# Optimization experiments

Hardware: AMD Instinct MI355X
Metric: run time of the kernel (lower is better)

The kernel has to match this reference:

```python
import jax, jax.numpy as jnp
import numpy as np

L, C, B = 256, 20, 1024


def _pos_mask(L):
    # pairwise mask: l2 - l1 >= 1, shape (L, L); broadcast over channels
    ls = jnp.arange(L)
    return (ls[None, :] - ls[:, None]) >= 1


def setup_inputs() -> dict:
    key = jax.random.key(0)
    k0, k1, k2 = jax.random.split(key, 3)
    x_lc = jax.random.uniform(k0, (B, L, C), dtype=jnp.float32)
    theta_0 = jnp.zeros((1,), dtype=jnp.float32)
    theta_lc = jax.random.normal(k1, (1, L, C), dtype=jnp.float32) / np.sqrt(L)
    pm = _pos_mask(L)
    theta_lclc = (jax.random.normal(k2, (1, L, C, L, C), dtype=jnp.float32)
                  / np.sqrt(L * L)) * pm[None, :, None, :, None]
    mask = pm
    return {"x_lc": x_lc, "theta_0": theta_0, "theta_lc": theta_lc,
            "theta_lclc": theta_lclc, "mask": mask}


def reference(x_lc, theta_0, theta_lc, theta_lclc, mask):
    Bn = x_lc.shape[0]
    # additive term: sum_{l,c} theta_lc * x
    phi = theta_0 + jnp.einsum('blc,zlc->b', x_lc, theta_lc)[:, None]
    # pairwise term as a masked bilinear form: x^T (mask * theta) x
    # (avoids materializing the (B,L,C,L,C) broadcast of the original)
    theta_m = theta_lclc[0] * mask[:, None, :, None].astype(theta_lclc.dtype)
    LC = L * C
    xf = x_lc.reshape(Bn, LC)                      # (B, LC)
    tf_ = theta_m.reshape(LC, LC)                  # (LC, LC)
    pair = jnp.einsum('bi,ij,bj->b', xf, tf_, xf)  # two GEMMs under the hood
    phi = phi + pair[:, None]
    return phi
```

## Files before the change

### kernel.cpp

```cpp
#include <hip/hip_runtime.h>
#include <stdint.h>

#define LDIM 256
#define CDIM 20
#define LC   5120
#define NB   1024
#define BM   256
#define BN   256
#define ITOT64 840

typedef __attribute__((ext_vector_type(8))) short short8;
typedef __attribute__((ext_vector_type(4))) float float4v;
typedef __attribute__((ext_vector_type(4))) unsigned int uint4v;
typedef unsigned short ushort_t;

#define TB_BYTES (52428800ull)
#define XB_BYTES (10485760ull)
#define WS_NEED  (TB_BYTES + XB_BYTES)

__device__ inline uint32_t pack_bf16x2(float a, float b) {
    uint32_t ua = __float_as_uint(a);
    uint32_t ub = __float_as_uint(b);
    ua += 0x7fffu + ((ua >> 16) & 1u);
    ub += 0x7fffu + ((ub >> 16) & 1u);
    return (ua >> 16) | (ub & 0xffff0000u);
}

__device__ inline float bf16_to_f32(ushort_t u) {
    return __uint_as_float(((uint32_t)u) << 16);
}

__device__ inline void load_lds16(const void* g, void* l) {
    __builtin_amdgcn_global_load_lds(
        (const __attribute__((address_space(1))) uint32_t*)g,
        (__attribute__((address_space(3))) uint32_t*)l, 16, 0, 0);
}

__global__ __launch_bounds__(256) void conv_kernel(
    const float* __restrict__ T, const float* __restrict__ X,
    const float* __restrict__ th0, const float* __restrict__ thlc,
    ushort_t* __restrict__ Tb, ushort_t* __restrict__ Xb,
    float* __restrict__ out)
{
    const int bid = blockIdx.x;
    const int t   = threadIdx.x;
    __shared__ float red[4];

    if (bid < LC) {
        const int r  = bid;
        const int tk = (r >> 8) << 8;
        const float*  src = T  + (size_t)r * LC;
        ushort_t*     dst = Tb + (size_t)r * LC;
        for (int c = tk + t * 4; c < LC; c += 1024) {
            float4 f = *(const float4*)(src + c);
            uint2 u;
            u.x = pack_bf16x2(f.x, f.y);
            u.y = pack_bf16x2(f.z, f.w);
            *(uint2*)(dst + c) = u;
        }
    } else {
        const int b = bid - LC;
        const float*  src = X  + (size_t)b * LC;
        ushort_t*     dst = Xb + (size_t)b * LC;
        float s = 0.f;
        for (int c = t * 4; c < LC; c += 1024) {
            float4 f = *(const float4*)(src + c);
            float4 w = *(const float4*)(thlc + c);
            s += f.x * w.x + f.y * w.y + f.z * w.z + f.w * w.w;
            uint2 u;
            u.x = pack_bf16x2(f.x, f.y);
            u.y = pack_bf16x2(f.z, f.w);
            *(uint2*)(dst + c) = u;
        }
        s += __shfl_xor(s, 1);  s += __shfl_xor(s, 2);  s += __shfl_xor(s, 4);
        s += __shfl_xor(s, 8);  s += __shfl_xor(s, 16); s += __shfl_xor(s, 32);
        if ((t & 63) == 0) red[t >> 6] = s;
        __syncthreads();
        if (t == 0) out[b] = th0[0] + red[0] + red[1] + red[2] + red[3];
    }
}

__global__ __launch_bounds__(512, 2) void pair_bf(
    const ushort_t* __restrict__ Tb, const ushort_t* __restrict__ Xb,
    float* __restrict__ out)
{
    const int n    = blockIdx.x;
    const int kblk = (n & 7) | ((n >> 5) << 3);
    const int bn0  = ((n >> 3) & 3) * BN;

    const int gbeg = (ITOT64 * kblk) >> 6;
    const int gend = (ITOT64 * (kblk + 1)) >> 6;

    int it = 0, pre = 0;
    while (pre + (80 - (it << 2)) <= gbeg) { pre += 80 - (it << 2); ++it; }
    int li = gbeg - pre;

    __shared__ __align__(16) ushort_t A_s[2048 * 8];
    __shared__ __align__(16) ushort_t B_s[2048 * 8];

    const int t    = threadIdx.x;
    const int lane = t & 63;
    const int wid  = t >> 6;
    const int wm   = (wid >> 1) * 64;
    const int wn   = (wid & 1) * 128;
    const int l16  = lane & 15;
    const int qk   = lane >> 4;

    uint32_t offA[4], offB[4];
    #pragma unroll
    for (int j = 0; j < 4; ++j) {
        const int c = (wid << 8) + (j << 6) + lane;
        const int row = c >> 3;
        const int g = (c & 7) ^ (row & 7);
        offA[j] = (uint32_t)row * LC + (g << 3);
        offB[j] = (uint32_t)(bn0 + row) * LC + (g << 3);
    }

    int adrA[2][4], adrB[2][8];
    #pragma unroll
    for (int step = 0; step < 2; ++step) {
        const int kf = step * 4 + qk;
        #pragma unroll
        for (int mt = 0; mt < 4; ++mt) {
            const int r = wm + mt * 16 + l16;
            adrA[step][mt] = ((r << 3) + (kf ^ (r & 7))) << 4;
        }
        #pragma unroll
        for (int nt = 0; nt < 8; ++nt) {
            const int r = wn + nt * 16 + l16;
            adrB[step][nt] = ((r << 3) + (kf ^ (r & 7))) << 4;
        }
    }

    int   i0    = it << 8;
    int   k0    = i0 + (li << 6);
    size_t baseA = (size_t)i0 * LC + k0;

    float4v acc[4][8];
    #pragma unroll
    for (int mt = 0; mt < 4; ++mt)
        #pragma unroll
        for (int nt = 0; nt < 8; ++nt)
            #pragma unroll
            for (int r = 0; r < 4; ++r) acc[mt][nt][r] = 0.f;

    for (int g = gbeg; g < gend; ++g) {
        __syncthreads();
        #pragma unroll
        for (int j = 0; j < 4; ++j)
            load_lds16(Tb + baseA + offA[j], A_s + (((wid << 8) + (j << 6)) << 3));
        #pragma unroll
        for (int j = 0; j < 4; ++j)
            load_lds16(Xb + k0 + offB[j],   B_s + (((wid << 8) + (j << 6)) << 3));
        __syncthreads();

        #pragma unroll
        for (int step = 0; step < 2; ++step) {
            short8 af[4], bfr[8];
            #pragma unroll
            for (int mt = 0; mt < 4; ++mt)
                af[mt] = *(const short8*)((const char*)A_s + adrA[step][mt]);
            #pragma unroll
            for (int nt = 0; nt < 8; ++nt)
                bfr[nt] = *(const short8*)((const char*)B_s + adrB[step][nt]);
            #pragma unroll
            for (int mt = 0; mt < 4; ++mt)
                #pragma unroll
                for (int nt = 0; nt < 8; ++nt)
                    acc[mt][nt] = __builtin_amdgcn_mfma_f32_16x16x32_bf16(
                        af[mt], bfr[nt], acc[mt][nt], 0, 0, 0);
        }

        ++li;
        const bool segEnd = (li == 80 - (it << 2));
        if (segEnd || g + 1 == gend) {
            #pragma unroll
            for (int nt = 0; nt < 8; ++nt) {
                const int b = bn0 + wn + nt * 16 + l16;
                const ushort_t* xb = Xb + (size_t)b * LC + i0 + wm + qk * 4;
                float s = 0.f;
                #pragma unroll
                for (int mt = 0; mt < 4; ++mt) {
                    ushort4 xv = *(const ushort4*)(xb + mt * 16);
                    s += acc[mt][nt][0] * bf16_to_f32(xv.x)
                       + acc[mt][nt][1] * bf16_to_f32(xv.y)
                       + acc[mt][nt][2] * bf16_to_f32(xv.z)
                       + acc[mt][nt][3] * bf16_to_f32(xv.w);
                }
                s += __shfl_xor(s, 16);
                s += __shfl_xor(s, 32);
                if (qk == 0) atomicAdd(&out[b], s);
            }
            #pragma unroll
            for (int mt = 0; mt < 4; ++mt)
                #pragma unroll
                for (int nt = 0; nt < 8; ++nt)
                    #pragma unroll
                    for (int r = 0; r < 4; ++r) acc[mt][nt][r] = 0.f;
        }
        if (segEnd) {
            ++it; li = 0;
            if (it < 20) {
                i0 = it << 8;
                k0 = i0;
                baseA = (size_t)i0 * LC + k0;
            }
        } else {
            k0 += 64;
            baseA += 64;
        }
    }
}

__global__ __launch_bounds__(256) void init_kernel(
    const float* __restrict__ x, const float* __restrict__ th0,
    const float* __restrict__ thlc, float* __restrict__ out)
{
    const int b = blockIdx.x;
    const float4* xb = (const float4*)(x + (size_t)b * LC);
    const float4* tv = (const float4*)thlc;
    float s = 0.f;
    for (int i = threadIdx.x; i < LC / 4; i += 256) {
        float4 a = xb[i], t = tv[i];
        s += a.x * t.x + a.y * t.y + a.z * t.z + a.w * t.w;
    }
    s += __shfl_xor(s, 1);  s += __shfl_xor(s, 2);  s += __shfl_xor(s, 4);
    s += __shfl_xor(s, 8);  s += __shfl_xor(s, 16); s += __shfl_xor(s, 32);
    __shared__ float red[4];
    if ((threadIdx.x & 63) == 0) red[threadIdx.x >> 6] = s;
    __syncthreads();
    if (threadIdx.x == 0) out[b] = th0[0] + red[0] + red[1] + red[2] + red[3];
}

__global__ __launch_bounds__(256) void pair_kernel(
    const float* __restrict__ T, const float* __restrict__ X,
    float* __restrict__ out)
{
    const int n  = blockIdx.x;
    const int r  = n & 7;
    const int g  = n >> 3;
    const int i0  = (g >> 3) * 128;
    const int bn0 = (g & 7) * 128;
    const int kstart = i0;
    const int nIter  = (LC - kstart) >> 6;
    const int ipc    = (nIter + 7) >> 3;
    const int itBeg  = r * ipc;
    const int itEnd  = (itBeg + ipc < nIter) ? (itBeg + ipc) : nIter;
    if (itBeg >= itEnd) return;
    const int kbeg   = kstart + (itBeg << 6);

    __shared__ __align__(16) short A_s[8 * 128 * 8];
    __shared__ __align__(16) short B_s[8 * 128 * 8];

    const int t    = threadIdx.x;
    const int lane = t & 63;
    const int wid  = t >> 6;
    const int wm   = (wid >> 1) * 64;
    const int wn   = (wid & 1) * 64;
    const int l16  = lane & 15;
    const int qk   = lane >> 4;

    const float* pA[4]; const float* pB[4]; int sIdx[4];
    #pragma unroll
    for (int u = 0; u < 4; ++u) {
        const int id  = t + u * 256;
        const int row = id >> 3;
        const int kq  = id & 7;
        pA[u] = T + (size_t)(i0 + row) * LC + kbeg + kq * 8;
        pB[u] = X + (size_t)(bn0 + row) * LC + kbeg + kq * 8;
        sIdx[u] = (kq * 128 + (row ^ kq)) * 8;
    }

    float4v acc[4][4] = {};
    for (int itr = itBeg; itr < itEnd; ++itr) {
        __syncthreads();
        #pragma unroll
        for (int u = 0; u < 4; ++u) {
            float4 a0 = ((const float4*)pA[u])[0];
            float4 a1 = ((const float4*)pA[u])[1];
            float4 b0 = ((const float4*)pB[u])[0];
            float4 b1 = ((const float4*)pB[u])[1];
            pA[u] += 64; pB[u] += 64;
            uint4v va, vb;
            va[0] = pack_bf16x2(a0.x, a0.y); va[1] = pack_bf16x2(a0.z, a0.w);
            va[2] = pack_bf16x2(a1.x, a1.y); va[3] = pack_bf16x2(a1.z, a1.w);
            vb[0] = pack_bf16x2(b0.x, b0.y); vb[1] = pack_bf16x2(b0.z, b0.w);
            vb[2] = pack_bf16x2(b1.x, b1.y); vb[3] = pack_bf16x2(b1.z, b1.w);
            *(uint4v*)(A_s + sIdx[u]) = va;
            *(uint4v*)(B_s + sIdx[u]) = vb;
        }
        __syncthreads();
        #pragma unroll
        for (int step = 0; step < 2; ++step) {
            const int kf = step * 4 + qk;
            short8 af[4], bfr[4];
            #pragma unroll
            for (int mt = 0; mt < 4; ++mt)
                af[mt] = *(const short8*)(A_s + (kf * 128 + ((wm + mt * 16 + l16) ^ kf)) * 8);
            #pragma unroll
            for (int nt = 0; nt < 4; ++nt)
                bfr[nt] = *(const short8*)(B_s + (kf * 128 + ((wn + nt * 16 + l16) ^ kf)) * 8);
            #pragma unroll
            for (int mt = 0; mt < 4; ++mt)
                #pragma unroll
                for (int nt = 0; nt < 4; ++nt)
                    acc[mt][nt] = __builtin_amdgcn_mfma_f32_16x16x32_bf16(
                        af[mt], bfr[nt], acc[mt][nt], 0, 0, 0);
        }
    }
    #pragma unroll
    for (int nt = 0; nt < 4; ++nt) {
        const int b = bn0 + wn + nt * 16 + l16;
        const float* xb = X + (size_t)b * LC + i0 + wm + qk * 4;
        float s = 0.f;
        #pragma unroll
        for (int mt = 0; mt < 4; ++mt) {
            float4 xv = *(const float4*)(xb + mt * 16);
            s += acc[mt][nt][0] * xv.x + acc[mt][nt][1] * xv.y +
                 acc[mt][nt][2] * xv.z + acc[mt][nt][3] * xv.w;
        }
        s += __shfl_xor(s, 16);
        s += __shfl_xor(s, 32);
        if (qk == 0) atomicAdd(&out[b], s);
    }
}

extern "C" void kernel_launch(void* const* d_in, const int* in_sizes, int n_in,
                              void* d_out, int out_size, void* d_ws, size_t ws_size,
                              hipStream_t stream) {
    const float* x    = (const float*)d_in[0];
    const float* th0  = (const float*)d_in[1];
    const float* thlc = (const float*)d_in[2];
    const float* T    = (const float*)d_in[3];
    float* out = (float*)d_out;

    if (ws_size >= WS_NEED) {
        ushort_t* Tb = (ushort_t*)d_ws;
        ushort_t* Xb = (ushort_t*)((char*)d_ws + TB_BYTES);
        conv_kernel<<<LC + NB, 256, 0, stream>>>(T, x, th0, thlc, Tb, Xb, out);
        pair_bf<<<256, 512, 0, stream>>>(Tb, Xb, out);
    } else {
        init_kernel<<<NB, 256, 0, stream>>>(x, th0, thlc, out);
        pair_kernel<<<(LC / 128) * (NB / 128) * 8, 256, 0, stream>>>(T, x, out);
    }
}
```

Baseline: 221.5 us.

## Double-buffer LDS tiles to prefetch the next K-slice during MFMA compute

```diff
diff --git a/kernel.cpp b/kernel.cpp
--- a/kernel.cpp
+++ b/kernel.cpp
@@ -93,10 +93,10 @@
 
     int it = 0, pre = 0;
     while (pre + (80 - (it << 2)) <= gbeg) { pre += 80 - (it << 2); ++it; }
-    int li = gbeg - pre;
-
-    __shared__ __align__(16) ushort_t A_s[2048 * 8];
-    __shared__ __align__(16) ushort_t B_s[2048 * 8];
+    const int li = gbeg - pre;
+
+    __shared__ __align__(16) ushort_t A_s[2][2048 * 8];
+    __shared__ __align__(16) ushort_t B_s[2][2048 * 8];
 
     const int t    = threadIdx.x;
     const int lane = t & 63;
@@ -132,9 +132,27 @@
         }
     }
 
-    int   i0    = it << 8;
-    int   k0    = i0 + (li << 6);
-    size_t baseA = (size_t)i0 * LC + k0;
+    int itI = it, liI = li;
+    int k0; size_t baseA;
+    auto rebaseI = [&]() {
+        const int i0I = itI << 8;
+        k0    = i0I + (liI << 6);
+        baseA = (size_t)i0I * LC + k0;
+    };
+    rebaseI();
+    auto issue = [&](int cb) {
+        #pragma unroll
+        for (int j = 0; j < 4; ++j)
+            load_lds16(Tb + baseA + offA[j], A_s[cb] + (((wid << 8) + (j << 6)) << 3));
+        #pragma unroll
+        for (int j = 0; j < 4; ++j)
+            load_lds16(Xb + k0 + offB[j],   B_s[cb] + (((wid << 8) + (j << 6)) << 3));
+        ++liI;
+        if (liI == 80 - (itI << 2)) {
+            ++itI; liI = 0;
+            if (itI < 20) rebaseI();
+        } else { k0 += 64; baseA += 64; }
+    };
 
     float4v acc[4][8];
     #pragma unroll
@@ -144,36 +162,40 @@
             #pragma unroll
             for (int r = 0; r < 4; ++r) acc[mt][nt][r] = 0.f;
 
+    int itC = it, liC = li;
+
+    issue(0);
+
     for (int g = gbeg; g < gend; ++g) {
+        const int cur = (g - gbeg) & 1;
         __syncthreads();
-        #pragma unroll
-        for (int j = 0; j < 4; ++j)
-            load_lds16(Tb + baseA + offA[j], A_s + (((wid << 8) + (j << 6)) << 3));
-        #pragma unroll
-        for (int j = 0; j < 4; ++j)
-            load_lds16(Xb + k0 + offB[j],   B_s + (((wid << 8) + (j << 6)) << 3));
-        __syncthreads();
-
-        #pragma unroll
-        for (int step = 0; step < 2; ++step) {
-            short8 af[4], bfr[8];
-            #pragma unroll
-            for (int mt = 0; mt < 4; ++mt)
-                af[mt] = *(const short8*)((const char*)A_s + adrA[step][mt]);
-            #pragma unroll
-            for (int nt = 0; nt < 8; ++nt)
-                bfr[nt] = *(const short8*)((const char*)B_s + adrB[step][nt]);
-            #pragma unroll
-            for (int mt = 0; mt < 4; ++mt)
+        if (g + 1 < gend) issue(cur ^ 1);
+
+        {
+            const ushort_t* As = A_s[cur];
+            const ushort_t* Bs = B_s[cur];
+            #pragma unroll
+            for (int step = 0; step < 2; ++step) {
+                short8 af[4], bfr[8];
+                #pragma unroll
+                for (int mt = 0; mt < 4; ++mt)
+                    af[mt] = *(const short8*)((const char*)As + adrA[step][mt]);
                 #pragma unroll
                 for (int nt = 0; nt < 8; ++nt)
-                    acc[mt][nt] = __builtin_amdgcn_mfma_f32_16x16x32_bf16(
-                        af[mt], bfr[nt], acc[mt][nt], 0, 0, 0);
-        }
-
-        ++li;
-        const bool segEnd = (li == 80 - (it << 2));
+                    bfr[nt] = *(const short8*)((const char*)Bs + adrB[step][nt]);
+                #pragma unroll
+                for (int mt = 0; mt < 4; ++mt)
+                    #pragma unroll
+                    for (int nt = 0; nt < 8; ++nt)
+                        acc[mt][nt] = __builtin_amdgcn_mfma_f32_16x16x32_bf16(
+                            af[mt], bfr[nt], acc[mt][nt], 0, 0, 0);
+            }
+        }
+
+        ++liC;
+        const bool segEnd = (liC == 80 - (itC << 2));
         if (segEnd || g + 1 == gend) {
+            const int i0 = itC << 8;
             #pragma unroll
             for (int nt = 0; nt < 8; ++nt) {
                 const int b = bn0 + wn + nt * 16 + l16;
@@ -198,17 +220,7 @@
                     #pragma unroll
                     for (int r = 0; r < 4; ++r) acc[mt][nt][r] = 0.f;
         }
-        if (segEnd) {
-            ++it; li = 0;
-            if (it < 20) {
-                i0 = it << 8;
-                k0 = i0;
-                baseA = (size_t)i0 * LC + k0;
-            }
-        } else {
-            k0 += 64;
-            baseA += 64;
-        }
+        if (segEnd) { ++itC; liC = 0; }
     }
 }
 
```

Measured after the change: 217.6 us. No clear change (-1.8%).
